# Performance work log

Hardware: AMD Instinct MI355X
Metric: run time of the kernel (lower is better)

The kernel has to match this reference:

```python
import jax, jax.numpy as jnp
import numpy as np

B, T, E, A = 512, 64, 1024, 32
S, D, H = 30, 200, 200          # stoch, deter, hidden
SS = D + S                      # state_size = 230
MIN_STD = 0.1
UPDATE_BIAS = -1.0
W_SCALE = 0.05


def setup_inputs() -> dict:
    key = jax.random.key(0)
    ks = jax.random.split(key, 17)
    n = jax.random.normal
    return {
        "embed":       n(ks[0], (B, T, E), jnp.float32),
        "action":      n(ks[1], (B, T, A), jnp.float32),
        "context":     n(ks[2], (B, T, SS), jnp.float32),
        "noise_prior": n(ks[3], (T, B, S), jnp.float32),
        "noise_post":  n(ks[4], (T, B, S), jnp.float32),
        "w_inp":       n(ks[5], (S + SS + A, H), jnp.float32) * W_SCALE,
        "b_inp":       jnp.zeros((H,), jnp.float32),
        "w_gru":       n(ks[6], (H + D, 3 * D), jnp.float32) * W_SCALE,
        "b_gru":       jnp.zeros((3 * D,), jnp.float32),
        "w_img_out":   n(ks[7], (D, H), jnp.float32) * W_SCALE,
        "b_img_out":   jnp.zeros((H,), jnp.float32),
        "w_obs_out":   n(ks[8], (D + E, H), jnp.float32) * W_SCALE,
        "b_obs_out":   jnp.zeros((H,), jnp.float32),
        "w_ims_stat":  n(ks[9], (H, 2 * S), jnp.float32) * W_SCALE,
        "b_ims_stat":  jnp.zeros((2 * S,), jnp.float32),
        "w_obs_stat":  n(ks[10], (H, 2 * S), jnp.float32) * W_SCALE,
        "b_obs_stat":  jnp.zeros((2 * S,), jnp.float32),
    }


def _observe(embed, action, context, noise_prior, noise_post,
             w_inp, b_inp, w_gru, b_gru, w_img_out, b_img_out,
             w_obs_out, b_obs_out, w_ims_stat, b_ims_stat,
             w_obs_stat, b_obs_stat):
    # time-major
    emb_t = jnp.swapaxes(embed, 0, 1)    # [T,B,E]
    act_t = jnp.swapaxes(action, 0, 1)   # [T,B,A]
    ctx_t = jnp.swapaxes(context, 0, 1)  # [T,B,SS]

    def step(carry, xs):
        stoch, deter = carry
        ctx, act, emb, n_p, n_o = xs
        # img_step: input MLP + GRU cell
        x = jnp.concatenate([stoch, ctx, act], -1)
        x = jax.nn.elu(x @ w_inp + b_inp)
        parts = jnp.concatenate([x, deter], -1) @ w_gru + b_gru
        reset, cand, update = jnp.split(parts, 3, -1)
        reset = jax.nn.sigmoid(reset)
        cand = jnp.tanh(reset * cand)
        update = jax.nn.sigmoid(update + UPDATE_BIAS)
        deter_new = update * cand + (1.0 - update) * deter
        # prior stats
        h = jax.nn.elu(deter_new @ w_img_out + b_img_out)
        st = h @ w_ims_stat + b_ims_stat
        pm, ps = jnp.split(st, 2, -1)
        ps = jax.nn.softplus(ps) + MIN_STD
        p_stoch = pm + ps * n_p
        # posterior stats
        ho = jax.nn.elu(jnp.concatenate([deter_new, emb], -1) @ w_obs_out + b_obs_out)
        so = ho @ w_obs_stat + b_obs_stat
        om, os_ = jnp.split(so, 2, -1)
        os_ = jax.nn.softplus(os_) + MIN_STD
        o_stoch = om + os_ * n_o
        out = jnp.concatenate([om, os_, o_stoch, pm, ps, p_stoch, deter_new], -1)
        return (o_stoch, deter_new), out

    carry0 = (jnp.zeros((B, S), embed.dtype), jnp.zeros((B, D), embed.dtype))
    _, ys = jax.lax.scan(step, carry0, (ctx_t, act_t, emb_t, noise_prior, noise_post))
    # ys: [T,B,6S+D] -> [B,T,6S+D]  (post mean/std/stoch, prior mean/std/stoch, deter)
    return jnp.swapaxes(ys, 0, 1)


def reference(embed, action, context, noise_prior, noise_post,
              w_inp, b_inp, w_gru, b_gru, w_img_out, b_img_out,
              w_obs_out, b_obs_out, w_ims_stat, b_ims_stat,
              w_obs_stat, b_obs_stat):
    return _observe(embed, action, context, noise_prior, noise_post,
                    w_inp, b_inp, w_gru, b_gru, w_img_out, b_img_out,
                    w_obs_out, b_obs_out, w_ims_stat, b_ims_stat,
                    w_obs_stat, b_obs_stat)
```

## Files before the change

### kernel.cpp

```cpp
#include <hip/hip_runtime.h>
#include <cstddef>

typedef short short8 __attribute__((ext_vector_type(8)));
typedef float f32x4 __attribute__((ext_vector_type(4)));
typedef unsigned short u16;

#define Bn 512
#define Tn 64
#define En 1024
#define An 32
#define Sn 30
#define Dn 200
#define Hn 200
#define SSn 230
#define OUTC 380

#define U16_WINP  0
#define EL_WINP   66560
#define U16_WGRU  66560
#define EL_WGRU   252928
#define U16_WIMG  319488
#define EL_WIMG   46592
#define U16_WOBSD 366080
#define EL_WOBSD  46592
#define U16_WIMS  412672
#define EL_WIMS   14336
#define U16_WOBSS 427008
#define EL_WOBSS  14336
#define U16_WOBSE 441344
#define EL_WOBSE  212992
#define U16_TOTAL 654336
#define PREOBS_BYTE_OFF 1308672

#define DEV static __device__ __forceinline__

DEV u16 f2bf(float f) {
  union { float f; unsigned u; } v; v.f = f;
  return (u16)((v.u + 0x7FFFu + ((v.u >> 16) & 1u)) >> 16);
}
DEV float bf2f(u16 h) {
  union { unsigned u; float f; } v; v.u = ((unsigned)h) << 16; return v.f;
}
DEV float elu1(float x)  { return x > 0.f ? x : expm1f(x); }
DEV float sigm(float x)  { return 1.f / (1.f + expf(-x)); }
DEV float splus(float x) { return x > 20.f ? x : log1pf(expf(x)); }

DEV void pack_one(const float* src, u16* dst, int li, int KT,
                  int Kr, int Nr, int ldN, int roff) {
  int j = li & 7, lane = (li >> 3) & 63, frag = li >> 9;
  int kt = frag % KT, nt = frag / KT;
  int k = kt * 32 + ((lane >> 4) << 3) + j;
  int n = nt * 16 + (lane & 15);
  float v = (k < Kr && n < Nr) ? src[(size_t)(k + roff) * ldN + n] : 0.f;
  dst[li] = f2bf(v);
}

__global__ __launch_bounds__(256) void k_pack(
    const float* w_inp, const float* w_gru, const float* w_img,
    const float* w_obs, const float* w_ims, const float* w_obss,
    u16* ws) {
  int idx = blockIdx.x * 256 + threadIdx.x;
  if (idx < U16_WGRU)       pack_one(w_inp,  ws + U16_WINP,  idx - U16_WINP, 10, 292, 200, 200, 0);
  else if (idx < U16_WIMG)  pack_one(w_gru,  ws + U16_WGRU,  idx - U16_WGRU, 13, 400, 600, 600, 0);
  else if (idx < U16_WOBSD) pack_one(w_img,  ws + U16_WIMG,  idx - U16_WIMG,  7, 200, 200, 200, 0);
  else if (idx < U16_WIMS)  pack_one(w_obs,  ws + U16_WOBSD, idx - U16_WOBSD, 7, 200, 200, 200, 0);
  else if (idx < U16_WOBSS) pack_one(w_ims,  ws + U16_WIMS,  idx - U16_WIMS,  7, 200,  60,  60, 0);
  else if (idx < U16_WOBSE) pack_one(w_obss, ws + U16_WOBSS, idx - U16_WOBSS, 7, 200,  60,  60, 0);
  else if (idx < U16_TOTAL) pack_one(w_obs,  ws + U16_WOBSE, idx - U16_WOBSE, 32, 1024, 200, 200, 200);
}

__global__ __launch_bounds__(256) void k_preobs(
    const float* __restrict__ emb, const u16* __restrict__ ws,
    float* __restrict__ pre) {
  __shared__ u16 Asm[64 * 72];
  __shared__ short8 Bsm[26 * 64];
  const short8* Wp = (const short8*)(ws + U16_WOBSE);

  int tid = threadIdx.x, wv = tid >> 6, lane = tid & 63;
  int lrow = lane & 15, quad = lane >> 4;
  int m0 = blockIdx.x * 64;
  int t = m0 >> 9, brow0 = m0 & 511;

  f32x4 acc[13];
  const f32x4 z4 = {0.f, 0.f, 0.f, 0.f};
#pragma unroll
  for (int i = 0; i < 13; ++i) acc[i] = z4;

  for (int kc = 0; kc < 16; ++kc) {
    __syncthreads();
#pragma unroll
    for (int q = 0; q < 4; ++q) {
      int i = tid + q * 256;
      int row = i >> 4, c4 = i & 15;
      const float* src = emb + ((size_t)((brow0 + row) * Tn + t)) * En + kc * 64 + c4 * 4;
      float4 v = *(const float4*)src;
      union { u16 h[4]; unsigned long long ll; } p;
      p.h[0] = f2bf(v.x); p.h[1] = f2bf(v.y); p.h[2] = f2bf(v.z); p.h[3] = f2bf(v.w);
      *(unsigned long long*)&Asm[row * 72 + c4 * 4] = p.ll;
    }
    for (int q = 0; q < 7; ++q) {
      int i = tid + q * 256;
      if (i < 1664) {
        int pair = i >> 6, l = i & 63;
        int ktl = pair / 13, nt = pair % 13;
        Bsm[i] = Wp[(nt * 32 + kc * 2 + ktl) * 64 + l];
      }
    }
    __syncthreads();
#pragma unroll
    for (int ktl = 0; ktl < 2; ++ktl) {
      short8 a = *(const short8*)&Asm[(wv * 16 + lrow) * 72 + ktl * 32 + quad * 8];
#pragma unroll
      for (int nt = 0; nt < 13; ++nt)
        acc[nt] = __builtin_amdgcn_mfma_f32_16x16x32_bf16(a, Bsm[(ktl * 13 + nt) * 64 + lane], acc[nt], 0, 0, 0);
    }
  }
#pragma unroll
  for (int nt = 0; nt < 13; ++nt) {
    int col = nt * 16 + lrow;
    if (col < 200) {
#pragma unroll
      for (int r = 0; r < 4; ++r) {
        int m = m0 + wv * 16 + quad * 4 + r;
        pre[(size_t)m * 200 + col] = acc[nt][r];
      }
    }
  }
}

__global__ __launch_bounds__(512, 2) void k_scan(
    const float* __restrict__ g_ctx, const float* __restrict__ g_act,
    const float* __restrict__ g_np, const float* __restrict__ g_no,
    const float* __restrict__ b_inp, const float* __restrict__ b_gru,
    const float* __restrict__ b_img, const float* __restrict__ b_obs,
    const float* __restrict__ b_ims, const float* __restrict__ b_obss,
    const u16* __restrict__ ws, const float* __restrict__ pre,
    float* __restrict__ out) {

  __shared__ u16 gin[16 * 424];
  __shared__ u16 U[16 * 616];
  __shared__ u16 hA[16 * 232];
  __shared__ u16 hoA[16 * 232];
  __shared__ float stp[16 * 66];
  __shared__ float sto[16 * 66];

  const short8* Winp  = (const short8*)(ws + U16_WINP);
  const short8* Wgru  = (const short8*)(ws + U16_WGRU);
  const short8* Wimg  = (const short8*)(ws + U16_WIMG);
  const short8* Wobsd = (const short8*)(ws + U16_WOBSD);
  const short8* Wims  = (const short8*)(ws + U16_WIMS);
  const short8* Wobss = (const short8*)(ws + U16_WOBSS);

  int tid = threadIdx.x, wv = tid >> 6, lane = tid & 63;
  int lrow = lane & 15, quad = lane >> 4;
  int b0 = blockIdx.x * 16;
  const f32x4 z4 = {0.f, 0.f, 0.f, 0.f};

  for (int i = tid; i < 16 * 424; i += 512) gin[i] = 0;
  for (int i = tid; i < 16 * 616; i += 512) U[i] = 0;
  for (int i = tid; i < 16 * 232; i += 512) { hA[i] = 0; hoA[i] = 0; }
  __syncthreads();

  for (int t = 0; t < Tn; ++t) {
    {
      int row = tid >> 5, sub = tid & 31;
      const float* crow = g_ctx + ((size_t)(b0 + row) * Tn + t) * SSn;
      for (int i = sub; i < SSn; i += 32) U[row * 328 + 30 + i] = f2bf(crow[i]);
      const float* arow = g_act + ((size_t)(b0 + row) * Tn + t) * An;
      if (sub < An) U[row * 328 + 260 + sub] = f2bf(arow[sub]);
      if (sub < 28) U[row * 328 + 292 + sub] = 0;
    }
    __syncthreads();

    for (int nt = wv; nt < 13; nt += 8) {
      f32x4 acc = z4;
      const short8* bp = Winp + (size_t)(nt * 10) * 64 + lane;
#pragma unroll
      for (int kt = 0; kt < 10; ++kt) {
        short8 a = *(const short8*)&U[lrow * 328 + kt * 32 + quad * 8];
        acc = __builtin_amdgcn_mfma_f32_16x16x32_bf16(a, bp[kt * 64], acc, 0, 0, 0);
      }
      int col = nt * 16 + lrow;
      if (col < 200) {
        float bias = b_inp[col];
#pragma unroll
        for (int r = 0; r < 4; ++r)
          gin[(quad * 4 + r) * 424 + col] = f2bf(elu1(acc[r] + bias));
      }
    }
    __syncthreads();

    for (int nt = wv; nt < 38; nt += 8) {
      f32x4 acc = z4;
      const short8* bp = Wgru + (size_t)(nt * 13) * 64 + lane;
#pragma unroll
      for (int kt = 0; kt < 13; ++kt) {
        short8 a = *(const short8*)&gin[lrow * 424 + kt * 32 + quad * 8];
        acc = __builtin_amdgcn_mfma_f32_16x16x32_bf16(a, bp[kt * 64], acc, 0, 0, 0);
      }
      int col = nt * 16 + lrow;
      if (col < 600) {
        float bias = b_gru[col];
#pragma unroll
        for (int r = 0; r < 4; ++r)
          U[(quad * 4 + r) * 616 + col] = f2bf(acc[r] + bias);
      }
    }
    __syncthreads();

    for (int i = tid; i < 16 * Dn; i += 512) {
      int row = i / Dn, d = i % Dn;
      float rg = bf2f(U[row * 616 + d]);
      float cg = bf2f(U[row * 616 + 200 + d]);
      float ug = bf2f(U[row * 616 + 400 + d]);
      float dold = bf2f(gin[row * 424 + 200 + d]);
      float rs  = sigm(rg);
      float cnd = tanhf(rs * cg);
      float up  = sigm(ug - 1.f);
      float dn  = up * cnd + (1.f - up) * dold;
      gin[row * 424 + 200 + d] = f2bf(dn);
      __builtin_nontemporal_store(dn, &out[((size_t)(b0 + row) * Tn + t) * OUTC + 180 + d]);
    }
    __syncthreads();

    for (int j = wv; j < 26; j += 8) {
      bool isobs = j >= 13;
      int nt = isobs ? j - 13 : j;
      const short8* bp = (isobs ? Wobsd : Wimg) + (size_t)(nt * 7) * 64 + lane;
      f32x4 acc = z4;
#pragma unroll
      for (int kt = 0; kt < 7; ++kt) {
        short8 a = *(const short8*)&gin[lrow * 424 + 200 + kt * 32 + quad * 8];
        acc = __builtin_amdgcn_mfma_f32_16x16x32_bf16(a, bp[kt * 64], acc, 0, 0, 0);
      }
      int col = nt * 16 + lrow;
      if (col < 200) {
        if (!isobs) {
          float bias = b_img[col];
#pragma unroll
          for (int r = 0; r < 4; ++r)
            hA[(quad * 4 + r) * 232 + col] = f2bf(elu1(acc[r] + bias));
        } else {
          float bias = b_obs[col];
#pragma unroll
          for (int r = 0; r < 4; ++r) {
            int row = quad * 4 + r;
            float po = pre[((size_t)t * Bn + b0 + row) * 200 + col];
            hoA[row * 232 + col] = f2bf(elu1(acc[r] + bias + po));
          }
        }
      }
    }
    __syncthreads();

    {
      bool isobs = wv >= 4;
      int nt = wv & 3;
      const short8* bp = (isobs ? Wobss : Wims) + (size_t)(nt * 7) * 64 + lane;
      const u16* src = isobs ? hoA : hA;
      f32x4 acc = z4;
#pragma unroll
      for (int kt = 0; kt < 7; ++kt) {
        short8 a = *(const short8*)&src[lrow * 232 + kt * 32 + quad * 8];
        acc = __builtin_amdgcn_mfma_f32_16x16x32_bf16(a, bp[kt * 64], acc, 0, 0, 0);
      }
      int col = nt * 16 + lrow;
      if (col < 60) {
        float bias = (isobs ? b_obss : b_ims)[col];
        float* dst = isobs ? sto : stp;
#pragma unroll
        for (int r = 0; r < 4; ++r)
          dst[(quad * 4 + r) * 66 + col] = acc[r] + bias;
      }
    }
    __syncthreads();

    if (tid < 480) {
      int row = tid / 30, s = tid % 30;
      size_t ob = ((size_t)(b0 + row) * Tn + t) * OUTC;
      size_t ni = ((size_t)t * Bn + b0 + row) * Sn + s;
      float pm = stp[row * 66 + s];
      float ps = splus(stp[row * 66 + 30 + s]) + 0.1f;
      float pst = pm + ps * g_np[ni];
      float om = sto[row * 66 + s];
      float os = splus(sto[row * 66 + 30 + s]) + 0.1f;
      float ost = om + os * g_no[ni];
      __builtin_nontemporal_store(om,  &out[ob + s]);
      __builtin_nontemporal_store(os,  &out[ob + 30 + s]);
      __builtin_nontemporal_store(ost, &out[ob + 60 + s]);
      __builtin_nontemporal_store(pm,  &out[ob + 90 + s]);
      __builtin_nontemporal_store(ps,  &out[ob + 120 + s]);
      __builtin_nontemporal_store(pst, &out[ob + 150 + s]);
      U[row * 328 + s] = f2bf(ost);
    }
    __syncthreads();
  }
}

extern "C" void kernel_launch(void* const* d_in, const int* in_sizes, int n_in,
                              void* d_out, int out_size, void* d_ws, size_t ws_size,
                              hipStream_t stream) {
  (void)in_sizes; (void)n_in; (void)out_size; (void)ws_size;
  const float* emb    = (const float*)d_in[0];
  const float* action = (const float*)d_in[1];
  const float* ctx    = (const float*)d_in[2];
  const float* np_    = (const float*)d_in[3];
  const float* no_    = (const float*)d_in[4];
  const float* w_inp  = (const float*)d_in[5];
  const float* b_inp  = (const float*)d_in[6];
  const float* w_gru  = (const float*)d_in[7];
  const float* b_gru  = (const float*)d_in[8];
  const float* w_img  = (const float*)d_in[9];
  const float* b_img  = (const float*)d_in[10];
  const float* w_obs  = (const float*)d_in[11];
  const float* b_obs  = (const float*)d_in[12];
  const float* w_ims  = (const float*)d_in[13];
  const float* b_ims  = (const float*)d_in[14];
  const float* w_obss = (const float*)d_in[15];
  const float* b_obss = (const float*)d_in[16];

  u16*   wsu = (u16*)d_ws;
  float* pre = (float*)((char*)d_ws + PREOBS_BYTE_OFF);
  float* out = (float*)d_out;

  k_pack<<<2556, 256, 0, stream>>>(w_inp, w_gru, w_img, w_obs, w_ims, w_obss, wsu);
  k_preobs<<<512, 256, 0, stream>>>(emb, wsu, pre);
  k_scan<<<32, 512, 0, stream>>>(ctx, action, np_, no_,
                                 b_inp, b_gru, b_img, b_obs, b_ims, b_obss,
                                 wsu, pre, out);
}
```

Baseline: 1.486 ms.

## Hoist input projections out of scan, move prior branch to parallel post-kernel

Precomputes the context/action part of the input MLP and the embed part of the posterior layer for all timesteps in a parallel pre-kernel, stored as bf16 with biases folded in. The recurrent scan keeps only the 30-wide stochastic input projection and fuses the GRU gate math into the GRU matmul epilogue, with interleaved weight packing and double-buffered state. The prior head, which does not feed the recurrence, is moved to a separate fully parallel kernel that reads deter back from the output. Uses fast exp2/rcp/log intrinsics and a coalesced packing kernel. This shortens the serial per-step critical path at the cost of extra global traffic and reduced-precision activations.

```diff
diff --git a/kernel.cpp b/kernel.cpp
--- a/kernel.cpp
+++ b/kernel.cpp
@@ -11,28 +11,31 @@
 #define An 32
 #define Sn 30
 #define Dn 200
-#define Hn 200
 #define SSn 230
 #define OUTC 380
 
-#define U16_WINP  0
-#define EL_WINP   66560
-#define U16_WGRU  66560
-#define EL_WGRU   252928
-#define U16_WIMG  319488
-#define EL_WIMG   46592
-#define U16_WOBSD 366080
-#define EL_WOBSD  46592
-#define U16_WIMS  412672
-#define EL_WIMS   14336
-#define U16_WOBSS 427008
-#define EL_WOBSS  14336
-#define U16_WOBSE 441344
-#define EL_WOBSE  212992
-#define U16_TOTAL 654336
-#define PREOBS_BYTE_OFF 1308672
+#define U16_WINP0  0
+#define U16_WINPCA 6656
+#define U16_WGRU   66560
+#define U16_WIMG   326144
+#define U16_WOBSD  372736
+#define U16_WIMS   419328
+#define U16_WOBSS  433664
+#define U16_WOBSE  448000
+#define U16_PREO   660992
+#define U16_PREI   7214592
+
+#define WINP0_8  0
+#define WINPCA_8 832
+#define WGRU_8   8320
+#define WIMG_8   40768
+#define WOBSD_8  46592
+#define WIMS_8   52416
+#define WOBSS_8  54208
+#define WOBSE_8  56000
 
 #define DEV static __device__ __forceinline__
+#define MFMA(a,b,c) __builtin_amdgcn_mfma_f32_16x16x32_bf16((a),(b),(c),0,0,0)
 
 DEV u16 f2bf(float f) {
   union { float f; unsigned u; } v; v.f = f;
@@ -41,58 +44,80 @@
 DEV float bf2f(u16 h) {
   union { unsigned u; float f; } v; v.u = ((unsigned)h) << 16; return v.f;
 }
-DEV float elu1(float x)  { return x > 0.f ? x : expm1f(x); }
-DEV float sigm(float x)  { return 1.f / (1.f + expf(-x)); }
-DEV float splus(float x) { return x > 20.f ? x : log1pf(expf(x)); }
-
-DEV void pack_one(const float* src, u16* dst, int li, int KT,
-                  int Kr, int Nr, int ldN, int roff) {
-  int j = li & 7, lane = (li >> 3) & 63, frag = li >> 9;
-  int kt = frag % KT, nt = frag / KT;
-  int k = kt * 32 + ((lane >> 4) << 3) + j;
-  int n = nt * 16 + (lane & 15);
-  float v = (k < Kr && n < Nr) ? src[(size_t)(k + roff) * ldN + n] : 0.f;
-  dst[li] = f2bf(v);
-}
-
-__global__ __launch_bounds__(256) void k_pack(
-    const float* w_inp, const float* w_gru, const float* w_img,
-    const float* w_obs, const float* w_ims, const float* w_obss,
-    u16* ws) {
-  int idx = blockIdx.x * 256 + threadIdx.x;
-  if (idx < U16_WGRU)       pack_one(w_inp,  ws + U16_WINP,  idx - U16_WINP, 10, 292, 200, 200, 0);
-  else if (idx < U16_WIMG)  pack_one(w_gru,  ws + U16_WGRU,  idx - U16_WGRU, 13, 400, 600, 600, 0);
-  else if (idx < U16_WOBSD) pack_one(w_img,  ws + U16_WIMG,  idx - U16_WIMG,  7, 200, 200, 200, 0);
-  else if (idx < U16_WIMS)  pack_one(w_obs,  ws + U16_WOBSD, idx - U16_WOBSD, 7, 200, 200, 200, 0);
-  else if (idx < U16_WOBSS) pack_one(w_ims,  ws + U16_WIMS,  idx - U16_WIMS,  7, 200,  60,  60, 0);
-  else if (idx < U16_WOBSE) pack_one(w_obss, ws + U16_WOBSS, idx - U16_WOBSS, 7, 200,  60,  60, 0);
-  else if (idx < U16_TOTAL) pack_one(w_obs,  ws + U16_WOBSE, idx - U16_WOBSE, 32, 1024, 200, 200, 200);
-}
-
-__global__ __launch_bounds__(256) void k_preobs(
-    const float* __restrict__ emb, const u16* __restrict__ ws,
-    float* __restrict__ pre) {
+DEV float fexp(float x)  { return __builtin_amdgcn_exp2f(x * 1.44269504f); }
+DEV float sigm(float x)  { return __builtin_amdgcn_rcpf(1.f + fexp(-x)); }
+DEV float tanhf_(float x){ return 1.f - 2.f * __builtin_amdgcn_rcpf(fexp(2.f * x) + 1.f); }
+DEV float elu1(float x)  { return x > 0.f ? x : fexp(x) - 1.f; }
+DEV float splus(float x) { return 0.69314718f * __builtin_amdgcn_logf(1.f + fexp(x)); }
+
+__global__ __launch_bounds__(256) void k_pack2(
+    const float* __restrict__ w_inp, const float* __restrict__ w_gru,
+    const float* __restrict__ w_img, const float* __restrict__ w_obs,
+    const float* __restrict__ w_ims, const float* __restrict__ w_obss,
+    u16* __restrict__ ws) {
+  int s = blockIdx.x;
+  const float* src; int KT, Kr, ldN, roff, colbase, cmax; size_t dstbase; int ntKT;
+  if (s < 13)      { src=w_inp;  KT=1;  Kr=30;   ldN=200; roff=0;   int nt=s;    colbase=nt*16; cmax=min(16,200-colbase); dstbase=U16_WINP0;  ntKT=nt*KT; }
+  else if (s < 26) { src=w_inp;  KT=9;  Kr=262;  ldN=200; roff=30;  int nt=s-13; colbase=nt*16; cmax=min(16,200-colbase); dstbase=U16_WINPCA; ntKT=nt*KT; }
+  else if (s < 65) { src=w_gru;  KT=13; Kr=400;  ldN=600; roff=0;   int ntp=s-26; int g=ntp/3, p=ntp%3;
+                     colbase=p*200+g*16; cmax=min(16,200-g*16); dstbase=U16_WGRU; ntKT=ntp*KT; }
+  else if (s < 78) { src=w_img;  KT=7;  Kr=200;  ldN=200; roff=0;   int nt=s-65; colbase=nt*16; cmax=min(16,200-colbase); dstbase=U16_WIMG;  ntKT=nt*KT; }
+  else if (s < 91) { src=w_obs;  KT=7;  Kr=200;  ldN=200; roff=0;   int nt=s-78; colbase=nt*16; cmax=min(16,200-colbase); dstbase=U16_WOBSD; ntKT=nt*KT; }
+  else if (s < 95) { src=w_ims;  KT=7;  Kr=200;  ldN=60;  roff=0;   int nt=s-91; colbase=nt*16; cmax=min(16,60-colbase);  dstbase=U16_WIMS;  ntKT=nt*KT; }
+  else if (s < 99) { src=w_obss; KT=7;  Kr=200;  ldN=60;  roff=0;   int nt=s-95; colbase=nt*16; cmax=min(16,60-colbase);  dstbase=U16_WOBSS; ntKT=nt*KT; }
+  else             { src=w_obs;  KT=32; Kr=1024; ldN=200; roff=200; int nt=s-99; colbase=nt*16; cmax=min(16,200-colbase); dstbase=U16_WOBSE; ntKT=nt*KT; }
+
+  __shared__ float Ws[2048];
+  int tid = threadIdx.x;
+  int nchunk = (KT + 3) >> 2;
+  for (int kc = 0; kc < nchunk; ++kc) {
+    __syncthreads();
+    for (int i = tid; i < 2048; i += 256) {
+      int r = i >> 4, c = i & 15;
+      int k = kc * 128 + r;
+      Ws[i] = (k < Kr && c < cmax) ? src[(size_t)(roff + k) * ldN + colbase + c] : 0.f;
+    }
+    __syncthreads();
+    int nf = KT - kc * 4; if (nf > 4) nf = 4;
+    int fi = tid >> 6, lane = tid & 63;
+    if (fi < nf) {
+      int kt = kc * 4 + fi;
+      union { u16 h[8]; short8 v; } pk;
+#pragma unroll
+      for (int j = 0; j < 8; ++j)
+        pk.h[j] = f2bf(Ws[(fi * 32 + ((lane >> 4) << 3) + j) * 16 + (lane & 15)]);
+      *(short8*)&ws[dstbase + (size_t)(ntKT + kt) * 512 + lane * 8] = pk.v;
+    }
+  }
+}
+
+__global__ __launch_bounds__(256) void k_pre(
+    const float* __restrict__ emb, const float* __restrict__ ctx,
+    const float* __restrict__ act, const float* __restrict__ b_obs,
+    const float* __restrict__ b_inp, u16* __restrict__ ws) {
   __shared__ u16 Asm[64 * 72];
   __shared__ short8 Bsm[26 * 64];
-  const short8* Wp = (const short8*)(ws + U16_WOBSE);
+  const short8* Wb = (const short8*)ws;
+  u16* preO = ws + U16_PREO;
+  u16* preI = ws + U16_PREI;
 
   int tid = threadIdx.x, wv = tid >> 6, lane = tid & 63;
   int lrow = lane & 15, quad = lane >> 4;
   int m0 = blockIdx.x * 64;
-  int t = m0 >> 9, brow0 = m0 & 511;
-
+  int t = m0 >> 9, b0 = m0 & 511;
+
+  const f32x4 z4 = {0.f, 0.f, 0.f, 0.f};
   f32x4 acc[13];
-  const f32x4 z4 = {0.f, 0.f, 0.f, 0.f};
+
 #pragma unroll
   for (int i = 0; i < 13; ++i) acc[i] = z4;
-
   for (int kc = 0; kc < 16; ++kc) {
     __syncthreads();
 #pragma unroll
     for (int q = 0; q < 4; ++q) {
       int i = tid + q * 256;
       int row = i >> 4, c4 = i & 15;
-      const float* src = emb + ((size_t)((brow0 + row) * Tn + t)) * En + kc * 64 + c4 * 4;
+      const float* src = emb + ((size_t)((b0 + row) * Tn + t)) * En + kc * 64 + c4 * 4;
       float4 v = *(const float4*)src;
       union { u16 h[4]; unsigned long long ll; } p;
       p.h[0] = f2bf(v.x); p.h[1] = f2bf(v.y); p.h[2] = f2bf(v.z); p.h[3] = f2bf(v.w);
@@ -103,7 +128,7 @@
       if (i < 1664) {
         int pair = i >> 6, l = i & 63;
         int ktl = pair / 13, nt = pair % 13;
-        Bsm[i] = Wp[(nt * 32 + kc * 2 + ktl) * 64 + l];
+        Bsm[i] = Wb[WOBSE_8 + (size_t)(nt * 32 + kc * 2 + ktl) * 64 + l];
       }
     }
     __syncthreads();
@@ -112,188 +137,320 @@
       short8 a = *(const short8*)&Asm[(wv * 16 + lrow) * 72 + ktl * 32 + quad * 8];
 #pragma unroll
       for (int nt = 0; nt < 13; ++nt)
-        acc[nt] = __builtin_amdgcn_mfma_f32_16x16x32_bf16(a, Bsm[(ktl * 13 + nt) * 64 + lane], acc[nt], 0, 0, 0);
+        acc[nt] = MFMA(a, Bsm[(ktl * 13 + nt) * 64 + lane], acc[nt]);
     }
   }
 #pragma unroll
   for (int nt = 0; nt < 13; ++nt) {
     int col = nt * 16 + lrow;
     if (col < 200) {
+      float bias = b_obs[col];
 #pragma unroll
       for (int r = 0; r < 4; ++r) {
-        int m = m0 + wv * 16 + quad * 4 + r;
-        pre[(size_t)m * 200 + col] = acc[nt][r];
+        int m = t * 512 + b0 + wv * 16 + quad * 4 + r;
+        preO[(size_t)m * 200 + col] = f2bf(acc[nt][r] + bias);
+      }
+    }
+  }
+
+#pragma unroll
+  for (int i = 0; i < 13; ++i) acc[i] = z4;
+  for (int kc = 0; kc < 5; ++kc) {
+    __syncthreads();
+#pragma unroll
+    for (int q = 0; q < 4; ++q) {
+      int i = tid + q * 256;
+      int row = i >> 4, c4 = i & 15;
+      union { u16 h[4]; unsigned long long ll; } p;
+#pragma unroll
+      for (int e = 0; e < 4; ++e) {
+        int k = kc * 64 + c4 * 4 + e;
+        float v = 0.f;
+        if (k < 230)      v = ctx[((size_t)(b0 + row) * Tn + t) * SSn + k];
+        else if (k < 262) v = act[((size_t)(b0 + row) * Tn + t) * An + (k - 230)];
+        p.h[e] = f2bf(v);
+      }
+      *(unsigned long long*)&Asm[row * 72 + c4 * 4] = p.ll;
+    }
+    int nktl = (kc < 4) ? 2 : 1;
+    for (int q = 0; q < 7; ++q) {
+      int i = tid + q * 256;
+      if (i < nktl * 13 * 64) {
+        int pair = i >> 6, l = i & 63;
+        int ktl = pair / 13, nt = pair % 13;
+        Bsm[i] = Wb[WINPCA_8 + (size_t)(nt * 9 + kc * 2 + ktl) * 64 + l];
+      }
+    }
+    __syncthreads();
+    for (int ktl = 0; ktl < nktl; ++ktl) {
+      short8 a = *(const short8*)&Asm[(wv * 16 + lrow) * 72 + ktl * 32 + quad * 8];
+#pragma unroll
+      for (int nt = 0; nt < 13; ++nt)
+        acc[nt] = MFMA(a, Bsm[(ktl * 13 + nt) * 64 + lane], acc[nt]);
+    }
+  }
+#pragma unroll
+  for (int nt = 0; nt < 13; ++nt) {
+    int col = nt * 16 + lrow;
+    if (col < 200) {
+      float bias = b_inp[col];
+#pragma unroll
+      for (int r = 0; r < 4; ++r) {
+        int m = t * 512 + b0 + wv * 16 + quad * 4 + r;
+        preI[(size_t)m * 200 + col] = f2bf(acc[nt][r] + bias);
       }
     }
   }
 }
 
 __global__ __launch_bounds__(512, 2) void k_scan(
-    const float* __restrict__ g_ctx, const float* __restrict__ g_act,
-    const float* __restrict__ g_np, const float* __restrict__ g_no,
-    const float* __restrict__ b_inp, const float* __restrict__ b_gru,
-    const float* __restrict__ b_img, const float* __restrict__ b_obs,
-    const float* __restrict__ b_ims, const float* __restrict__ b_obss,
-    const u16* __restrict__ ws, const float* __restrict__ pre,
+    const float* __restrict__ g_no, const float* __restrict__ b_gru,
+    const float* __restrict__ b_obss, const u16* __restrict__ ws,
     float* __restrict__ out) {
 
-  __shared__ u16 gin[16 * 424];
-  __shared__ u16 U[16 * 616];
-  __shared__ u16 hA[16 * 232];
+  __shared__ u16 AB[16 * 872];
+  __shared__ u16 Uin[16 * 40];
   __shared__ u16 hoA[16 * 232];
-  __shared__ float stp[16 * 66];
   __shared__ float sto[16 * 66];
 
-  const short8* Winp  = (const short8*)(ws + U16_WINP);
-  const short8* Wgru  = (const short8*)(ws + U16_WGRU);
-  const short8* Wimg  = (const short8*)(ws + U16_WIMG);
-  const short8* Wobsd = (const short8*)(ws + U16_WOBSD);
-  const short8* Wims  = (const short8*)(ws + U16_WIMS);
-  const short8* Wobss = (const short8*)(ws + U16_WOBSS);
+  const short8* Wb = (const short8*)ws;
+  const u16* preO = ws + U16_PREO;
+  const u16* preI = ws + U16_PREI;
+
+  const int tid = threadIdx.x, wv = tid >> 6, lane = tid & 63;
+  const int lrow = lane & 15, quad = lane >> 4;
+  const int b0 = blockIdx.x * 16;
+  const f32x4 z4 = {0.f, 0.f, 0.f, 0.f};
+
+  const bool two = wv < 5;
+  const int colA0 = wv * 16 + lrow;
+  const int colA1 = (wv + 8) * 16 + lrow;
+  const int dcol0 = colA0;
+  const int dcol1 = colA1;
+  const int nrow = tid / 30, ns = tid - nrow * 30;
+
+  short8 fA0 = Wb[WINP0_8 + (size_t)wv * 64 + lane];
+  short8 fA1 = two ? Wb[WINP0_8 + (size_t)(wv + 8) * 64 + lane] : fA0;
+
+  float bgr0 = b_gru[dcol0], bgc0 = b_gru[200 + dcol0], bgu0 = b_gru[400 + dcol0];
+  float bgr1 = 0.f, bgc1 = 0.f, bgu1 = 0.f;
+  if (two && dcol1 < 200) { bgr1 = b_gru[dcol1]; bgc1 = b_gru[200 + dcol1]; bgu1 = b_gru[400 + dcol1]; }
+  const int cD = (wv & 3) * 16 + lrow;
+  const float bD = (wv < 4 && cD < 60) ? b_obss[cD] : 0.f;
+
+  for (int i = tid; i < 16 * 872; i += 512) AB[i] = 0;
+  for (int i = tid; i < 16 * 40; i += 512) Uin[i] = 0;
+  for (int i = tid; i < 16 * 232; i += 512) hoA[i] = 0;
+  __syncthreads();
+
+  for (int t = 0; t < Tn; ++t) {
+    const int par = t & 1;
+    const int pb = par * 424, qb = 424 - pb;
+
+    u16 pin0[4], pin1[4] = {0,0,0,0}, pob0[4], pob1[4] = {0,0,0,0};
+    {
+      size_t mb = (size_t)t * 512 + b0 + quad * 4;
+#pragma unroll
+      for (int r = 0; r < 4; ++r) pin0[r] = preI[(mb + r) * 200 + colA0];
+      if (two && colA1 < 200) {
+#pragma unroll
+        for (int r = 0; r < 4; ++r) pin1[r] = preI[(mb + r) * 200 + colA1];
+      }
+#pragma unroll
+      for (int r = 0; r < 4; ++r) pob0[r] = preO[(mb + r) * 200 + colA0];
+      if (two && colA1 < 200) {
+#pragma unroll
+        for (int r = 0; r < 4; ++r) pob1[r] = preO[(mb + r) * 200 + colA1];
+      }
+    }
+    float vno = 0.f;
+    if (tid < 480) vno = g_no[((size_t)t * 512 + b0 + nrow) * Sn + ns];
+
+    __syncthreads();
+
+    {
+      short8 aU = *(const short8*)&Uin[lrow * 40 + quad * 8];
+      f32x4 a0 = MFMA(aU, fA0, z4);
+#pragma unroll
+      for (int r = 0; r < 4; ++r)
+        AB[(quad * 4 + r) * 872 + pb + colA0] = f2bf(elu1(a0[r] + bf2f(pin0[r])));
+      if (two) {
+        f32x4 a1 = MFMA(aU, fA1, z4);
+        if (colA1 < 200) {
+#pragma unroll
+          for (int r = 0; r < 4; ++r)
+            AB[(quad * 4 + r) * 872 + pb + colA1] = f2bf(elu1(a1[r] + bf2f(pin1[r])));
+        }
+      }
+    }
+    __syncthreads();
+
+    {
+      short8 ax[13];
+#pragma unroll
+      for (int kt = 0; kt < 13; ++kt)
+        ax[kt] = *(const short8*)&AB[lrow * 872 + pb + kt * 32 + quad * 8];
+      const int ng = two ? 2 : 1;
+      for (int gi = 0; gi < ng; ++gi) {
+        int g = wv + 8 * gi;
+        int dcol = gi ? dcol1 : dcol0;
+        float br = gi ? bgr1 : bgr0, bc = gi ? bgc1 : bgc0, bu = gi ? bgu1 : bgu0;
+        const short8* bpr = Wb + WGRU_8 + (size_t)((3 * g + 0) * 13) * 64 + lane;
+        const short8* bpc = Wb + WGRU_8 + (size_t)((3 * g + 1) * 13) * 64 + lane;
+        const short8* bpu = Wb + WGRU_8 + (size_t)((3 * g + 2) * 13) * 64 + lane;
+        f32x4 ar = z4, ac = z4, au = z4;
+#pragma unroll
+        for (int kt = 0; kt < 13; ++kt) ar = MFMA(ax[kt], bpr[kt * 64], ar);
+#pragma unroll
+        for (int kt = 0; kt < 13; ++kt) ac = MFMA(ax[kt], bpc[kt * 64], ac);
+#pragma unroll
+        for (int kt = 0; kt < 13; ++kt) au = MFMA(ax[kt], bpu[kt * 64], au);
+        if (dcol < 200) {
+#pragma unroll
+          for (int r = 0; r < 4; ++r) {
+            int row = quad * 4 + r;
+            float dold = bf2f(AB[row * 872 + pb + 200 + dcol]);
+            float rs = sigm(ar[r] + br);
+            float cnd = tanhf_(rs * (ac[r] + bc));
+            float up = sigm(au[r] + bu - 1.f);
+            float dn = up * cnd + (1.f - up) * dold;
+            AB[row * 872 + qb + 200 + dcol] = f2bf(dn);
+            __builtin_nontemporal_store(dn, &out[((size_t)(b0 + row) * Tn + t) * OUTC + 180 + dcol]);
+          }
+        }
+      }
+    }
+    __syncthreads();
+
+    {
+      short8 ad[7];
+#pragma unroll
+      for (int kt = 0; kt < 7; ++kt)
+        ad[kt] = *(const short8*)&AB[lrow * 872 + qb + 200 + kt * 32 + quad * 8];
+      {
+        const short8* bp = Wb + WOBSD_8 + (size_t)(wv * 7) * 64 + lane;
+        f32x4 a0 = z4;
+#pragma unroll
+        for (int kt = 0; kt < 7; ++kt) a0 = MFMA(ad[kt], bp[kt * 64], a0);
+#pragma unroll
+        for (int r = 0; r < 4; ++r)
+          hoA[(quad * 4 + r) * 232 + colA0] = f2bf(elu1(a0[r] + bf2f(pob0[r])));
+      }
+      if (two && colA1 < 200) {
+        const short8* bp = Wb + WOBSD_8 + (size_t)((wv + 8) * 7) * 64 + lane;
+        f32x4 a1 = z4;
+#pragma unroll
+        for (int kt = 0; kt < 7; ++kt) a1 = MFMA(ad[kt], bp[kt * 64], a1);
+#pragma unroll
+        for (int r = 0; r < 4; ++r)
+          hoA[(quad * 4 + r) * 232 + colA1] = f2bf(elu1(a1[r] + bf2f(pob1[r])));
+      }
+    }
+    __syncthreads();
+
+    if (wv < 4) {
+      const short8* bp = Wb + WOBSS_8 + (size_t)(wv * 7) * 64 + lane;
+      f32x4 acc = z4;
+#pragma unroll
+      for (int kt = 0; kt < 7; ++kt) {
+        short8 a = *(const short8*)&hoA[lrow * 232 + kt * 32 + quad * 8];
+        acc = MFMA(a, bp[kt * 64], acc);
+      }
+      if (cD < 60) {
+#pragma unroll
+        for (int r = 0; r < 4; ++r) sto[(quad * 4 + r) * 66 + cD] = acc[r] + bD;
+      }
+    }
+    __syncthreads();
+
+    if (tid < 480) {
+      size_t ob = ((size_t)(b0 + nrow) * Tn + t) * OUTC;
+      float om = sto[nrow * 66 + ns];
+      float os = splus(sto[nrow * 66 + 30 + ns]) + 0.1f;
+      float ost = om + os * vno;
+      __builtin_nontemporal_store(om,  &out[ob + ns]);
+      __builtin_nontemporal_store(os,  &out[ob + 30 + ns]);
+      __builtin_nontemporal_store(ost, &out[ob + 60 + ns]);
+      Uin[nrow * 40 + ns] = f2bf(ost);
+    }
+  }
+}
+
+__global__ __launch_bounds__(256) void k_prior(
+    const float* __restrict__ g_np, const float* __restrict__ b_img,
+    const float* __restrict__ b_ims, const u16* __restrict__ ws,
+    float* __restrict__ out) {
+  __shared__ u16 Ad[64 * 232];
+  __shared__ u16 Ah[64 * 232];
+  __shared__ float stf[64 * 66];
+  const short8* Wb = (const short8*)ws;
 
   int tid = threadIdx.x, wv = tid >> 6, lane = tid & 63;
   int lrow = lane & 15, quad = lane >> 4;
-  int b0 = blockIdx.x * 16;
+  int b = blockIdx.x;
   const f32x4 z4 = {0.f, 0.f, 0.f, 0.f};
 
-  for (int i = tid; i < 16 * 424; i += 512) gin[i] = 0;
-  for (int i = tid; i < 16 * 616; i += 512) U[i] = 0;
-  for (int i = tid; i < 16 * 232; i += 512) { hA[i] = 0; hoA[i] = 0; }
+  for (int i = tid; i < 64 * 232; i += 256) { Ad[i] = 0; Ah[i] = 0; }
   __syncthreads();
 
-  for (int t = 0; t < Tn; ++t) {
-    {
-      int row = tid >> 5, sub = tid & 31;
-      const float* crow = g_ctx + ((size_t)(b0 + row) * Tn + t) * SSn;
-      for (int i = sub; i < SSn; i += 32) U[row * 328 + 30 + i] = f2bf(crow[i]);
-      const float* arow = g_act + ((size_t)(b0 + row) * Tn + t) * An;
-      if (sub < An) U[row * 328 + 260 + sub] = f2bf(arow[sub]);
-      if (sub < 28) U[row * 328 + 292 + sub] = 0;
-    }
-    __syncthreads();
-
-    for (int nt = wv; nt < 13; nt += 8) {
+  for (int idx = tid; idx < 64 * 200; idx += 256) {
+    int row = idx / 200, col = idx - row * 200;
+    Ad[row * 232 + col] = f2bf(out[((size_t)b * Tn + row) * OUTC + 180 + col]);
+  }
+  __syncthreads();
+
+  {
+    short8 af[7];
+#pragma unroll
+    for (int kt = 0; kt < 7; ++kt)
+      af[kt] = *(const short8*)&Ad[(wv * 16 + lrow) * 232 + kt * 32 + quad * 8];
+    for (int nt = 0; nt < 13; ++nt) {
+      const short8* bp = Wb + WIMG_8 + (size_t)(nt * 7) * 64 + lane;
       f32x4 acc = z4;
-      const short8* bp = Winp + (size_t)(nt * 10) * 64 + lane;
-#pragma unroll
-      for (int kt = 0; kt < 10; ++kt) {
-        short8 a = *(const short8*)&U[lrow * 328 + kt * 32 + quad * 8];
-        acc = __builtin_amdgcn_mfma_f32_16x16x32_bf16(a, bp[kt * 64], acc, 0, 0, 0);
-      }
+#pragma unroll
+      for (int kt = 0; kt < 7; ++kt) acc = MFMA(af[kt], bp[kt * 64], acc);
       int col = nt * 16 + lrow;
       if (col < 200) {
-        float bias = b_inp[col];
+        float bias = b_img[col];
 #pragma unroll
         for (int r = 0; r < 4; ++r)
-          gin[(quad * 4 + r) * 424 + col] = f2bf(elu1(acc[r] + bias));
-      }
-    }
-    __syncthreads();
-
-    for (int nt = wv; nt < 38; nt += 8) {
+          Ah[(wv * 16 + quad * 4 + r) * 232 + col] = f2bf(elu1(acc[r] + bias));
+      }
+    }
+  }
+  __syncthreads();
+
+  {
+    short8 ah[7];
+#pragma unroll
+    for (int kt = 0; kt < 7; ++kt)
+      ah[kt] = *(const short8*)&Ah[(wv * 16 + lrow) * 232 + kt * 32 + quad * 8];
+#pragma unroll
+    for (int nt = 0; nt < 4; ++nt) {
+      const short8* bp = Wb + WIMS_8 + (size_t)(nt * 7) * 64 + lane;
       f32x4 acc = z4;
-      const short8* bp = Wgru + (size_t)(nt * 13) * 64 + lane;
-#pragma unroll
-      for (int kt = 0; kt < 13; ++kt) {
-        short8 a = *(const short8*)&gin[lrow * 424 + kt * 32 + quad * 8];
-        acc = __builtin_amdgcn_mfma_f32_16x16x32_bf16(a, bp[kt * 64], acc, 0, 0, 0);
-      }
-      int col = nt * 16 + lrow;
-      if (col < 600) {
-        float bias = b_gru[col];
-#pragma unroll
-        for (int r = 0; r < 4; ++r)
-          U[(quad * 4 + r) * 616 + col] = f2bf(acc[r] + bias);
-      }
-    }
-    __syncthreads();
-
-    for (int i = tid; i < 16 * Dn; i += 512) {
-      int row = i / Dn, d = i % Dn;
-      float rg = bf2f(U[row * 616 + d]);
-      float cg = bf2f(U[row * 616 + 200 + d]);
-      float ug = bf2f(U[row * 616 + 400 + d]);
-      float dold = bf2f(gin[row * 424 + 200 + d]);
-      float rs  = sigm(rg);
-      float cnd = tanhf(rs * cg);
-      float up  = sigm(ug - 1.f);
-      float dn  = up * cnd + (1.f - up) * dold;
-      gin[row * 424 + 200 + d] = f2bf(dn);
-      __builtin_nontemporal_store(dn, &out[((size_t)(b0 + row) * Tn + t) * OUTC + 180 + d]);
-    }
-    __syncthreads();
-
-    for (int j = wv; j < 26; j += 8) {
-      bool isobs = j >= 13;
-      int nt = isobs ? j - 13 : j;
-      const short8* bp = (isobs ? Wobsd : Wimg) + (size_t)(nt * 7) * 64 + lane;
-      f32x4 acc = z4;
-#pragma unroll
-      for (int kt = 0; kt < 7; ++kt) {
-        short8 a = *(const short8*)&gin[lrow * 424 + 200 + kt * 32 + quad * 8];
-        acc = __builtin_amdgcn_mfma_f32_16x16x32_bf16(a, bp[kt * 64], acc, 0, 0, 0);
-      }
-      int col = nt * 16 + lrow;
-      if (col < 200) {
-        if (!isobs) {
-          float bias = b_img[col];
-#pragma unroll
-          for (int r = 0; r < 4; ++r)
-            hA[(quad * 4 + r) * 232 + col] = f2bf(elu1(acc[r] + bias));
-        } else {
-          float bias = b_obs[col];
-#pragma unroll
-          for (int r = 0; r < 4; ++r) {
-            int row = quad * 4 + r;
-            float po = pre[((size_t)t * Bn + b0 + row) * 200 + col];
-            hoA[row * 232 + col] = f2bf(elu1(acc[r] + bias + po));
-          }
-        }
-      }
-    }
-    __syncthreads();
-
-    {
-      bool isobs = wv >= 4;
-      int nt = wv & 3;
-      const short8* bp = (isobs ? Wobss : Wims) + (size_t)(nt * 7) * 64 + lane;
-      const u16* src = isobs ? hoA : hA;
-      f32x4 acc = z4;
-#pragma unroll
-      for (int kt = 0; kt < 7; ++kt) {
-        short8 a = *(const short8*)&src[lrow * 232 + kt * 32 + quad * 8];
-        acc = __builtin_amdgcn_mfma_f32_16x16x32_bf16(a, bp[kt * 64], acc, 0, 0, 0);
-      }
+#pragma unroll
+      for (int kt = 0; kt < 7; ++kt) acc = MFMA(ah[kt], bp[kt * 64], acc);
       int col = nt * 16 + lrow;
       if (col < 60) {
-        float bias = (isobs ? b_obss : b_ims)[col];
-        float* dst = isobs ? sto : stp;
+        float bias = b_ims[col];
 #pragma unroll
         for (int r = 0; r < 4; ++r)
-          dst[(quad * 4 + r) * 66 + col] = acc[r] + bias;
-      }
-    }
-    __syncthreads();
-
-    if (tid < 480) {
-      int row = tid / 30, s = tid % 30;
-      size_t ob = ((size_t)(b0 + row) * Tn + t) * OUTC;
-      size_t ni = ((size_t)t * Bn + b0 + row) * Sn + s;
-      float pm = stp[row * 66 + s];
-      float ps = splus(stp[row * 66 + 30 + s]) + 0.1f;
-      float pst = pm + ps * g_np[ni];
-      float om = sto[row * 66 + s];
-      float os = splus(sto[row * 66 + 30 + s]) + 0.1f;
-      float ost = om + os * g_no[ni];
-      __builtin_nontemporal_store(om,  &out[ob + s]);
-      __builtin_nontemporal_store(os,  &out[ob + 30 + s]);
-      __builtin_nontemporal_store(ost, &out[ob + 60 + s]);
-      __builtin_nontemporal_store(pm,  &out[ob + 90 + s]);
-      __builtin_nontemporal_store(ps,  &out[ob + 120 + s]);
-      __builtin_nontemporal_store(pst, &out[ob + 150 + s]);
-      U[row * 328 + s] = f2bf(ost);
-    }
-    __syncthreads();
+          stf[(wv * 16 + quad * 4 + r) * 66 + col] = acc[r] + bias;
+      }
+    }
+  }
+  __syncthreads();
+
+  for (int idx = tid; idx < 64 * 30; idx += 256) {
+    int row = idx / 30, s = idx - row * 30;
+    float pm = stf[row * 66 + s];
+    float ps = splus(stf[row * 66 + 30 + s]) + 0.1f;
+    float pst = pm + ps * g_np[((size_t)row * 512 + b) * Sn + s];
+    size_t ob = ((size_t)b * Tn + row) * OUTC;
+    __builtin_nontemporal_store(pm,  &out[ob + 90 + s]);
+    __builtin_nontemporal_store(ps,  &out[ob + 120 + s]);
+    __builtin_nontemporal_store(pst, &out[ob + 150 + s]);
   }
 }
 
@@ -319,13 +476,11 @@
   const float* w_obss = (const float*)d_in[15];
   const float* b_obss = (const float*)d_in[16];
 
-  u16*   wsu = (u16*)d_ws;
-  float* pre = (float*)((char*)d_ws + PREOBS_BYTE_OFF);
+  u16* wsu = (u16*)d_ws;
   float* out = (float*)d_out;
 
-  k_pack<<<2556, 256, 0, stream>>>(w_inp, w_gru, w_img, w_obs, w_ims, w_obss, wsu);
-  k_preobs<<<512, 256, 0, stream>>>(emb, wsu, pre);
-  k_scan<<<32, 512, 0, stream>>>(ctx, action, np_, no_,
-                                 b_inp, b_gru, b_img, b_obs, b_ims, b_obss,
-                                 wsu, pre, out);
-}
+  k_pack2<<<112, 256, 0, stream>>>(w_inp, w_gru, w_img, w_obs, w_ims, w_obss, wsu);
+  k_pre<<<512, 256, 0, stream>>>(emb, ctx, action, b_obs, b_inp, wsu);
+  k_scan<<<32, 512, 0, stream>>>(no_, b_gru, b_obss, wsu, out);
+  k_prior<<<512, 256, 0, stream>>>(np_, b_img, b_ims, wsu, out);
+}
```

Result: faster. 1.227 ms (-17.4%).
